# Kernel optimization log

Hardware: AMD Instinct MI355X
Metric: run time of the kernel (lower is better)

The kernel has to match this reference:

```python
import jax, jax.numpy as jnp
import numpy as np

THRESHOLDS = (0.25, 0.375, 0.5, 0.625)
NUM_CLASSES = 5
SMOOTH = 1e-5  # dice smoothing constant


def setup_inputs() -> dict:
    key = jax.random.key(0)
    k1, k2 = jax.random.split(key)
    # [N, T, C, H, W]; input has 5 class channels, target 1 intensity channel
    inp = jax.random.uniform(k1, (4, 10, 5, 384, 384), dtype=jnp.float32)
    tgt = jax.random.uniform(k2, (4, 10, 1, 384, 384), dtype=jnp.float32)
    weight = jnp.array([1.0, 1.0, 2.0, 5.0, 10.0], dtype=jnp.float32)
    return {"input": inp, "target": tgt, "weight": weight}


def reference(input, target, weight):
    # permute to [N, C, T, H, W]
    x = jnp.transpose(input, (0, 2, 1, 3, 4))   # [N,5,T,H,W]
    t = jnp.transpose(target, (0, 2, 1, 3, 4))  # [N,1,T,H,W]
    # threshold binning: class index = number of thresholds <= target value
    cls = jnp.zeros(t.shape, dtype=jnp.int32)
    for thr in THRESHOLDS:
        cls = cls + (t >= thr).astype(jnp.int32)
    # one-hot scatter along class dim -> [N,5,T,H,W]
    class_ids = jnp.arange(NUM_CLASSES, dtype=jnp.int32).reshape(1, NUM_CLASSES, 1, 1, 1)
    onehot = (cls == class_ids).astype(x.dtype)
    # per-class dice over all remaining dims
    axes = (0, 2, 3, 4)
    inter = jnp.sum(x * onehot, axis=axes)                      # [5]
    denom = jnp.sum(x, axis=axes) + jnp.sum(onehot, axis=axes)  # [5]
    dice_loss = 1.0 - (2.0 * inter + SMOOTH) / (denom + SMOOTH)  # [5]
    return jnp.sum(weight * dice_loss)
```

## Files before the change

kernel.cpp:

```cpp
#include <hip/hip_runtime.h>

#define HW      147456
#define NC      5
#define NGROUP  1474560
#define NBLK    1440
#define SMOOTH  1e-5f

__global__ __launch_bounds__(256) void dice_main(const float* __restrict__ inp,
                                                 const float* __restrict__ tgt,
                                                 float* __restrict__ part) {
    float sumx[NC]  = {0.f, 0.f, 0.f, 0.f, 0.f};
    float inter[NC] = {0.f, 0.f, 0.f, 0.f, 0.f};
    float cnt[NC]   = {0.f, 0.f, 0.f, 0.f, 0.f};

    const int tid    = blockIdx.x * 256 + threadIdx.x;
    const int stride = gridDim.x * 256;

    for (int g = tid; g < NGROUP; g += stride) {
        const int p  = g << 2;
        const int nt = p / HW;
        const int hw = p - nt * HW;

        const float4 t4 = reinterpret_cast<const float4*>(tgt)[g];
        const int c0 = (t4.x >= 0.25f) + (t4.x >= 0.375f) + (t4.x >= 0.5f) + (t4.x >= 0.625f);
        const int c1 = (t4.y >= 0.25f) + (t4.y >= 0.375f) + (t4.y >= 0.5f) + (t4.y >= 0.625f);
        const int c2 = (t4.z >= 0.25f) + (t4.z >= 0.375f) + (t4.z >= 0.5f) + (t4.z >= 0.625f);
        const int c3 = (t4.w >= 0.25f) + (t4.w >= 0.375f) + (t4.w >= 0.5f) + (t4.w >= 0.625f);

        const float* base = inp + (size_t)nt * (size_t)(NC * HW) + (size_t)hw;
        #pragma unroll
        for (int c = 0; c < NC; ++c) {
            const float4 x4 = *reinterpret_cast<const float4*>(base + (size_t)c * HW);
            sumx[c] += (x4.x + x4.y) + (x4.z + x4.w);
            float iv = 0.f;
            if (c0 == c) iv += x4.x;
            if (c1 == c) iv += x4.y;
            if (c2 == c) iv += x4.z;
            if (c3 == c) iv += x4.w;
            inter[c] += iv;
            cnt[c]   += (float)((c0 == c) + (c1 == c) + (c2 == c) + (c3 == c));
        }
    }

    float v[15];
    #pragma unroll
    for (int c = 0; c < NC; ++c) { v[c] = sumx[c]; v[5 + c] = inter[c]; v[10 + c] = cnt[c]; }

    #pragma unroll
    for (int j = 0; j < 15; ++j) {
        #pragma unroll
        for (int off = 32; off > 0; off >>= 1)
            v[j] += __shfl_down(v[j], off, 64);
    }

    __shared__ float sm[4][15];
    const int lane = threadIdx.x & 63;
    const int wv   = threadIdx.x >> 6;
    if (lane == 0) {
        #pragma unroll
        for (int j = 0; j < 15; ++j) sm[wv][j] = v[j];
    }
    __syncthreads();
    if (threadIdx.x < 16) {
        float s = 0.f;
        if (threadIdx.x < 15)
            s = sm[0][threadIdx.x] + sm[1][threadIdx.x] +
                sm[2][threadIdx.x] + sm[3][threadIdx.x];
        part[blockIdx.x * 16 + threadIdx.x] = s;
    }
}

__global__ __launch_bounds__(256) void dice_reduce(const float* __restrict__ part,
                                                   const float* __restrict__ w,
                                                   float* __restrict__ out) {
    const int j  = threadIdx.x & 15;
    const int rg = threadIdx.x >> 4;
    float s = 0.f;
    for (int r = rg; r < NBLK; r += 16)
        s += part[r * 16 + j];

    __shared__ float sm[16][17];
    __shared__ float tot[16];
    sm[rg][j] = s;
    __syncthreads();
    if (threadIdx.x < 16) {
        float t = 0.f;
        #pragma unroll
        for (int k = 0; k < 16; ++k) t += sm[k][threadIdx.x];
        tot[threadIdx.x] = t;
    }
    __syncthreads();
    if (threadIdx.x == 0) {
        float loss = 0.f;
        #pragma unroll
        for (int c = 0; c < NC; ++c) {
            const float inter = tot[5 + c];
            const float denom = tot[c] + tot[10 + c];
            loss += w[c] * (1.f - (2.f * inter + SMOOTH) / (denom + SMOOTH));
        }
        out[0] = loss;
    }
}

extern "C" void kernel_launch(void* const* d_in, const int* in_sizes, int n_in,
                              void* d_out, int out_size, void* d_ws, size_t ws_size,
                              hipStream_t stream) {
    const float* inp = (const float*)d_in[0];
    const float* tgt = (const float*)d_in[1];
    const float* wgt = (const float*)d_in[2];
    float* out = (float*)d_out;
    float* ws  = (float*)d_ws;

    dice_main<<<NBLK, 256, 0, stream>>>(inp, tgt, ws);
    dice_reduce<<<1, 256, 0, stream>>>(ws, wgt, out);
}
```

Before: 209.4 us.

## Replace grid-stride loop with one-shot 2D grid and unroll final reduction

The main kernel drops its grid-stride loop. It now launches a 2D grid of 144x40 blocks, each thread handling exactly one float4 group, so there is no per-iteration integer division and all five loads are issued at once. This exposes more memory-level parallelism. In exchange, four times as many blocks each do a full 15-value shuffle reduction and write partials, and the single-block final reduction has four times as many partials to sum, so that loop is unrolled by four.

```diff
diff --git a/kernel.cpp b/kernel.cpp
--- a/kernel.cpp
+++ b/kernel.cpp
@@ -2,49 +2,45 @@
 
 #define HW      147456
 #define NC      5
-#define NGROUP  1474560
-#define NBLK    1440
+#define NT      40
+#define GX      144
+#define NBLK    (GX * NT)
 #define SMOOTH  1e-5f
 
 __global__ __launch_bounds__(256) void dice_main(const float* __restrict__ inp,
                                                  const float* __restrict__ tgt,
                                                  float* __restrict__ part) {
-    float sumx[NC]  = {0.f, 0.f, 0.f, 0.f, 0.f};
-    float inter[NC] = {0.f, 0.f, 0.f, 0.f, 0.f};
-    float cnt[NC]   = {0.f, 0.f, 0.f, 0.f, 0.f};
+    const int nt = blockIdx.y;
+    const int hw = (blockIdx.x * 256 + threadIdx.x) << 2;
 
-    const int tid    = blockIdx.x * 256 + threadIdx.x;
-    const int stride = gridDim.x * 256;
+    const float4 t4 = *reinterpret_cast<const float4*>(tgt + (size_t)nt * HW + hw);
 
-    for (int g = tid; g < NGROUP; g += stride) {
-        const int p  = g << 2;
-        const int nt = p / HW;
-        const int hw = p - nt * HW;
+    const float* base = inp + (size_t)nt * (NC * HW) + hw;
+    const float4 x0 = *reinterpret_cast<const float4*>(base);
+    const float4 x1 = *reinterpret_cast<const float4*>(base + HW);
+    const float4 x2 = *reinterpret_cast<const float4*>(base + 2 * HW);
+    const float4 x3 = *reinterpret_cast<const float4*>(base + 3 * HW);
+    const float4 x4 = *reinterpret_cast<const float4*>(base + 4 * HW);
 
-        const float4 t4 = reinterpret_cast<const float4*>(tgt)[g];
-        const int c0 = (t4.x >= 0.25f) + (t4.x >= 0.375f) + (t4.x >= 0.5f) + (t4.x >= 0.625f);
-        const int c1 = (t4.y >= 0.25f) + (t4.y >= 0.375f) + (t4.y >= 0.5f) + (t4.y >= 0.625f);
-        const int c2 = (t4.z >= 0.25f) + (t4.z >= 0.375f) + (t4.z >= 0.5f) + (t4.z >= 0.625f);
-        const int c3 = (t4.w >= 0.25f) + (t4.w >= 0.375f) + (t4.w >= 0.5f) + (t4.w >= 0.625f);
+    const int c0 = (t4.x >= 0.25f) + (t4.x >= 0.375f) + (t4.x >= 0.5f) + (t4.x >= 0.625f);
+    const int c1 = (t4.y >= 0.25f) + (t4.y >= 0.375f) + (t4.y >= 0.5f) + (t4.y >= 0.625f);
+    const int c2 = (t4.z >= 0.25f) + (t4.z >= 0.375f) + (t4.z >= 0.5f) + (t4.z >= 0.625f);
+    const int c3 = (t4.w >= 0.25f) + (t4.w >= 0.375f) + (t4.w >= 0.5f) + (t4.w >= 0.625f);
 
-        const float* base = inp + (size_t)nt * (size_t)(NC * HW) + (size_t)hw;
-        #pragma unroll
-        for (int c = 0; c < NC; ++c) {
-            const float4 x4 = *reinterpret_cast<const float4*>(base + (size_t)c * HW);
-            sumx[c] += (x4.x + x4.y) + (x4.z + x4.w);
-            float iv = 0.f;
-            if (c0 == c) iv += x4.x;
-            if (c1 == c) iv += x4.y;
-            if (c2 == c) iv += x4.z;
-            if (c3 == c) iv += x4.w;
-            inter[c] += iv;
-            cnt[c]   += (float)((c0 == c) + (c1 == c) + (c2 == c) + (c3 == c));
-        }
-    }
-
+    const float4 xs[NC] = {x0, x1, x2, x3, x4};
     float v[15];
     #pragma unroll
-    for (int c = 0; c < NC; ++c) { v[c] = sumx[c]; v[5 + c] = inter[c]; v[10 + c] = cnt[c]; }
+    for (int c = 0; c < NC; ++c) {
+        const float4 x = xs[c];
+        v[c] = (x.x + x.y) + (x.z + x.w);
+        float iv = 0.f;
+        if (c0 == c) iv += x.x;
+        if (c1 == c) iv += x.y;
+        if (c2 == c) iv += x.z;
+        if (c3 == c) iv += x.w;
+        v[5 + c]  = iv;
+        v[10 + c] = (float)((c0 == c) + (c1 == c) + (c2 == c) + (c3 == c));
+    }
 
     #pragma unroll
     for (int j = 0; j < 15; ++j) {
@@ -66,7 +62,7 @@
         if (threadIdx.x < 15)
             s = sm[0][threadIdx.x] + sm[1][threadIdx.x] +
                 sm[2][threadIdx.x] + sm[3][threadIdx.x];
-        part[blockIdx.x * 16 + threadIdx.x] = s;
+        part[(blockIdx.y * GX + blockIdx.x) * 16 + threadIdx.x] = s;
     }
 }
 
@@ -75,9 +71,14 @@
                                                    float* __restrict__ out) {
     const int j  = threadIdx.x & 15;
     const int rg = threadIdx.x >> 4;
-    float s = 0.f;
-    for (int r = rg; r < NBLK; r += 16)
-        s += part[r * 16 + j];
+    float s0 = 0.f, s1 = 0.f, s2 = 0.f, s3 = 0.f;
+    for (int r = rg; r < NBLK; r += 64) {
+        s0 += part[(r)      * 16 + j];
+        s1 += part[(r + 16) * 16 + j];
+        s2 += part[(r + 32) * 16 + j];
+        s3 += part[(r + 48) * 16 + j];
+    }
+    const float s = (s0 + s1) + (s2 + s3);
 
     __shared__ float sm[16][17];
     __shared__ float tot[16];
@@ -111,6 +112,7 @@
     float* out = (float*)d_out;
     float* ws  = (float*)d_ws;
 
-    dice_main<<<NBLK, 256, 0, stream>>>(inp, tgt, ws);
+    dim3 grid(GX, NT);
+    dice_main<<<grid, 256, 0, stream>>>(inp, tgt, ws);
     dice_reduce<<<1, 256, 0, stream>>>(ws, wgt, out);
 }
```

Result: no change. 211.4 us (+1.0%).
